# Optimization experiments

Measured on AMD Instinct MI355X. Metric: run time of the kernel, lower is better.

Reference implementation:

```python
import jax, jax.numpy as jnp
import numpy as np
import math

HIDDEN = 384
HEADS = 4
HEAD_DIM = HIDDEN // HEADS
B, T = 8, 2048


def _shift_rel(pos_tensor):
    # pos_tensor: [b, h, t, 2t-1] -> [b, h, t, t] (Transformer-XL shift trick)
    b, h, t, n = pos_tensor.shape
    zero_pad = jnp.zeros((b, h, t, 1), dtype=pos_tensor.dtype)
    padded = jnp.concatenate([zero_pad, pos_tensor], axis=-1)  # [b,h,t,n+1]
    padded = padded.reshape(b, h, n + 1, t)
    shifted = padded[:, :, 1:].reshape(b, h, t, n)
    return shifted[:, :, :, : n // 2 + 1]  # [b,h,t,t]


def setup_inputs() -> dict:
    key = jax.random.key(0)
    ks = jax.random.split(key, 12)
    s = 1.0 / math.sqrt(HIDDEN)
    inp = {
        "hidden_states": jax.random.normal(ks[0], (B, T, HIDDEN), jnp.float32),
        "pos_emb": jax.random.normal(ks[1], (1, 2 * T - 1, HIDDEN), jnp.float32),
        "attention_mask": jnp.ones((B, 1, T), jnp.int32),
        "Wq": jax.random.normal(ks[2], (HIDDEN, HIDDEN), jnp.float32) * s,
        "bq": jnp.zeros((HIDDEN,), jnp.float32),
        "Wk": jax.random.normal(ks[3], (HIDDEN, HIDDEN), jnp.float32) * s,
        "bk": jnp.zeros((HIDDEN,), jnp.float32),
        "Wv": jax.random.normal(ks[4], (HIDDEN, HIDDEN), jnp.float32) * s,
        "bv": jnp.zeros((HIDDEN,), jnp.float32),
        "Wo": jax.random.normal(ks[5], (HIDDEN, HIDDEN), jnp.float32) * s,
        "bo": jnp.zeros((HIDDEN,), jnp.float32),
        "Wpos": jax.random.normal(ks[6], (HIDDEN, HIDDEN), jnp.float32) * s,
        "pos_bias_u": jax.random.normal(ks[7], (HEADS, HEAD_DIM), jnp.float32) * s,
        "pos_bias_v": jax.random.normal(ks[8], (HEADS, HEAD_DIM), jnp.float32) * s,
    }
    return inp


def reference(hidden_states, pos_emb, attention_mask, Wq, bq, Wk, bk, Wv, bv,
              Wo, bo, Wpos, pos_bias_u, pos_bias_v):
    bsz, q_len, _ = hidden_states.shape
    # projections (nn.Linear applies x @ W.T + b; weights here stored as [in, out])
    q = (hidden_states @ Wq + bq).reshape(bsz, q_len, HEADS, HEAD_DIM)
    k = (hidden_states @ Wk + bk).reshape(bsz, q_len, HEADS, HEAD_DIM)
    v = (hidden_states @ Wv + bv).reshape(bsz, q_len, HEADS, HEAD_DIM)
    pos = (pos_emb @ Wpos).reshape(pos_emb.shape[0], -1, HEADS, HEAD_DIM)

    q_u = (q + pos_bias_u).transpose(0, 2, 1, 3)  # [b,h,t,d]
    q_v = (q + pos_bias_v).transpose(0, 2, 1, 3)

    # content score: [b,h,t,t]
    matrix_ac = jnp.einsum('bhqd,bkhd->bhqk', q_u, k)
    # position score: [b,h,t,2t-1] then shift
    matrix_bd = jnp.einsum('bhqd,pnhd->bhqn', q_v, pos)
    matrix_bd = _shift_rel(matrix_bd)

    scores = (matrix_ac + matrix_bd) / math.sqrt(HEAD_DIM)

    mask = (attention_mask[:, None] == 0)  # [b,1,1,t]
    min_val = jnp.finfo(scores.dtype).min
    scores = jnp.where(mask, min_val, scores)
    attn = jax.nn.softmax(scores, axis=-1)
    attn = jnp.where(mask, 0.0, attn)

    out = jnp.einsum('bhqk,bkhd->bqhd', attn, v).reshape(bsz, q_len, HIDDEN)
    return out @ Wo + bo
```

## Files before the change

kernel.cpp:

```cpp
#include <hip/hip_runtime.h>
#include <hip/hip_bf16.h>

#define TSEQ 2048
#define HID 384
#define NHEAD 4
#define HD 96
#define NBATCH 8

using bf16 = __bf16;
typedef bf16 bf16x8 __attribute__((ext_vector_type(8)));
typedef bf16 bf16x4 __attribute__((ext_vector_type(4)));
typedef float f32x4 __attribute__((ext_vector_type(4)));

static __device__ __forceinline__ f32x4 mfma16(bf16x8 a, bf16x8 b, f32x4 c) {
    return __builtin_amdgcn_mfma_f32_16x16x32_bf16(a, b, c, 0, 0, 0);
}

__global__ void k_conv8(const float* __restrict__ src, bf16* __restrict__ dst, int n8) {
    int t = blockIdx.x * 256 + threadIdx.x;
    if (t >= n8) return;
    const float4* s4 = reinterpret_cast<const float4*>(src);
    float4 a = s4[2 * t], b = s4[2 * t + 1];
    bf16x8 o;
    o[0] = (bf16)a.x; o[1] = (bf16)a.y; o[2] = (bf16)a.z; o[3] = (bf16)a.w;
    o[4] = (bf16)b.x; o[5] = (bf16)b.y; o[6] = (bf16)b.z; o[7] = (bf16)b.w;
    *reinterpret_cast<bf16x8*>(dst + 8 * t) = o;
}

__global__ void k_convT(const float* __restrict__ W, bf16* __restrict__ WT) {
    int t = blockIdx.x * 256 + threadIdx.x;
    int n = t / HID, k = t % HID;
    WT[t] = (bf16)W[(size_t)k * HID + n];
}

__launch_bounds__(256, 2)
__global__ void k_proj(const bf16* __restrict__ X, const bf16* __restrict__ P,
                       const bf16* __restrict__ wqT, const bf16* __restrict__ wkT,
                       const bf16* __restrict__ wvT, const bf16* __restrict__ wpT,
                       const float* __restrict__ bq, const float* __restrict__ bk,
                       const float* __restrict__ bv,
                       const float* __restrict__ pbu, const float* __restrict__ pbv,
                       bf16* __restrict__ qu, bf16* __restrict__ qv,
                       bf16* __restrict__ kws, bf16* __restrict__ vt,
                       bf16* __restrict__ pp) {
    __shared__ bf16 wt_lds[96][392];
    const float SC = 0.10206207262f;
    int mat = blockIdx.z;
    int m0 = blockIdx.x * 64;
    if (mat == 3 && m0 >= 4095) return;
    int n0 = blockIdx.y * 96;
    const bf16* A  = (mat == 3) ? P : X;
    const bf16* WT = (mat == 0) ? wqT : (mat == 1) ? wkT : (mat == 2) ? wvT : wpT;
    int tid = threadIdx.x;
    #pragma unroll
    for (int s = 0; s < 18; ++s) {
        int cc = tid + 256 * s;
        int r = cc / 48, ch = cc % 48;
        *reinterpret_cast<int4*>(&wt_lds[r][ch * 8]) =
            *reinterpret_cast<const int4*>(WT + (size_t)(n0 + r) * HID + ch * 8);
    }
    __syncthreads();
    int lane = tid & 63, w = tid >> 6;
    int c = lane & 15, g = lane >> 4;
    int arow = m0 + 16 * w + c;
    if (mat == 3 && arow > 4095) arow = 4095;
    const bf16* Abase = A + (size_t)arow * HID + 8 * g;
    f32x4 acc[6] = {};
    for (int ks = 0; ks < 12; ++ks) {
        bf16x8 a = *reinterpret_cast<const bf16x8*>(Abase + 32 * ks);
        #pragma unroll
        for (int jt = 0; jt < 6; ++jt) {
            bf16x8 b = *reinterpret_cast<const bf16x8*>(&wt_lds[16 * jt + c][32 * ks + 8 * g]);
            acc[jt] = mfma16(a, b, acc[jt]);
        }
    }
    int h = blockIdx.y;
    int rbase = m0 + 16 * w + 4 * g;
    if (mat == 0) {
        #pragma unroll
        for (int jt = 0; jt < 6; ++jt) {
            int n = n0 + 16 * jt + c;
            int d = 16 * jt + c;
            float bb = bq[n], bu = pbu[n], bvv = pbv[n];
            #pragma unroll
            for (int j = 0; j < 4; ++j) {
                int m = rbase + j;
                int b_ = m >> 11, t = m & 2047;
                size_t o = (((size_t)(b_ * NHEAD + h)) * TSEQ + t) * HD + d;
                float q = acc[jt][j] + bb;
                qu[o] = (bf16)((q + bu) * SC);
                qv[o] = (bf16)((q + bvv) * SC);
            }
        }
    } else if (mat == 1) {
        #pragma unroll
        for (int jt = 0; jt < 6; ++jt) {
            int n = n0 + 16 * jt + c;
            int d = 16 * jt + c;
            float bb = bk[n];
            #pragma unroll
            for (int j = 0; j < 4; ++j) {
                int m = rbase + j;
                int b_ = m >> 11, t = m & 2047;
                size_t o = (((size_t)(b_ * NHEAD + h)) * TSEQ + t) * HD + d;
                kws[o] = (bf16)(acc[jt][j] + bb);
            }
        }
    } else if (mat == 2) {
        #pragma unroll
        for (int jt = 0; jt < 6; ++jt) {
            int d = 16 * jt + c;
            float bb = bv[n0 + 16 * jt + c];
            int m = rbase;
            int b_ = m >> 11, t0 = m & 2047;
            size_t o = (((size_t)(b_ * NHEAD + h)) * HD + d) * TSEQ + t0;
            bf16x4 pk;
            #pragma unroll
            for (int j = 0; j < 4; ++j) pk[j] = (bf16)(acc[jt][j] + bb);
            *reinterpret_cast<bf16x4*>(vt + o) = pk;
        }
    } else {
        #pragma unroll
        for (int jt = 0; jt < 6; ++jt) {
            int d = 16 * jt + c;
            #pragma unroll
            for (int j = 0; j < 4; ++j) {
                int m = rbase + j;
                if (m < 4095) {
                    size_t o = ((size_t)h * 4096 + m) * HD + d;
                    pp[o] = (bf16)acc[jt][j];
                }
            }
        }
    }
}

__launch_bounds__(256, 4)
__global__ void k_attn(const bf16* __restrict__ qu, const bf16* __restrict__ qv,
                       const bf16* __restrict__ kws, const bf16* __restrict__ vt,
                       const bf16* __restrict__ pp, const int* __restrict__ mask,
                       bf16* __restrict__ out) {
    __shared__ bf16 k_lds[64][104];
    __shared__ bf16 vt_lds[96][64];
    __shared__ bf16 wp_lds[4][16][104];
    __shared__ float msk_lds[64];

    int bid = blockIdx.x;
    int x = bid & 7, j5 = bid >> 3;
    int h = x & 3;
    int b_ = (x >> 2) * 4 + (j5 >> 5);
    int qb = j5 & 31;
    int bh = b_ * NHEAD + h;
    int q0 = qb * 64;

    int tid = threadIdx.x, lane = tid & 63, w = tid >> 6;
    int c = lane & 15, g = lane >> 4;
    const int n_base0 = TSEQ - 1 - 63 - q0;
    const float L2E = 1.44269504089f;
    int sw = 48 - 16 * w;

    int cc0 = tid, cc1 = tid + 256, cc2 = tid + 512;
    int kr0 = cc0 / 12, kc0 = cc0 % 12;
    int kr1 = cc1 / 12, kc1 = cc1 % 12;
    int kr2 = cc2 / 12, kc2 = cc2 % 12;
    int vr0 = cc0 >> 3, vc0 = cc0 & 7;
    int vr1 = cc1 >> 3, vc1 = cc1 & 7;
    int vr2 = cc2 >> 3, vc2 = cc2 & 7;
    int kO0 = kr0 * HD + kc0 * 8, kO1 = kr1 * HD + kc1 * 8, kO2 = kr2 * HD + kc2 * 8;
    int vO0 = vr0 * TSEQ + vc0 * 8, vO1 = vr1 * TSEQ + vc1 * 8, vO2 = vr2 * TSEQ + vc2 * 8;
    bf16* kP0 = &k_lds[kr0][kc0 * 8];
    bf16* kP1 = &k_lds[kr1][kc1 * 8];
    bf16* kP2 = &k_lds[kr2][kc2 * 8];
    bf16* vP0 = &vt_lds[vr0][(vc0 ^ (vr0 & 7)) * 8];
    bf16* vP1 = &vt_lds[vr1][(vc1 ^ (vr1 & 7)) * 8];
    bf16* vP2 = &vt_lds[vr2][(vc2 ^ (vr2 & 7)) * 8];

    const bf16* kbP = kws + (size_t)bh * TSEQ * HD;
    const bf16* vbP = vt + (size_t)bh * HD * TSEQ;
    const bf16* pbP = pp + (size_t)h * 4096 * HD;
    const int*  mbP = mask + b_ * TSEQ;

    bf16x8 qu_f[3], qv_f[3];
    {
        size_t rowbase = ((size_t)bh * TSEQ + q0 + 16 * w + c) * HD + 8 * g;
        #pragma unroll
        for (int ds = 0; ds < 3; ++ds) {
            qu_f[ds] = *reinterpret_cast<const bf16x8*>(qu + rowbase + 32 * ds);
            qv_f[ds] = *reinterpret_cast<const bf16x8*>(qv + rowbase + 32 * ds);
        }
    }

    f32x4 acc_o[6] = {};
    float mrow = -3.0e38f, lrow = 0.f;

    {
        *reinterpret_cast<int4*>(kP0) = *reinterpret_cast<const int4*>(kbP + kO0);
        *reinterpret_cast<int4*>(kP1) = *reinterpret_cast<const int4*>(kbP + kO1);
        *reinterpret_cast<int4*>(kP2) = *reinterpret_cast<const int4*>(kbP + kO2);
        *reinterpret_cast<int4*>(vP0) = *reinterpret_cast<const int4*>(vbP + vO0);
        *reinterpret_cast<int4*>(vP1) = *reinterpret_cast<const int4*>(vbP + vO1);
        *reinterpret_cast<int4*>(vP2) = *reinterpret_cast<const int4*>(vbP + vO2);
        if (tid < 64) msk_lds[tid] = (mbP[tid] == 0) ? -1e30f : 0.f;
    }
    __syncthreads();

    for (int kt = 0; kt < 32; ++kt) {
        int wbase = n_base0 + 64 * kt + sw;
        {
            f32x4 w0 = {}, w1 = {};
            const bf16* p0 = pbP + (size_t)(wbase + c) * HD + 8 * g;
            const bf16* p1 = pbP + (size_t)(wbase + 16 + c) * HD + 8 * g;
            #pragma unroll
            for (int ds = 0; ds < 3; ++ds) {
                w0 = mfma16(*reinterpret_cast<const bf16x8*>(p0 + 32 * ds), qv_f[ds], w0);
                w1 = mfma16(*reinterpret_cast<const bf16x8*>(p1 + 32 * ds), qv_f[ds], w1);
            }
            #pragma unroll
            for (int j = 0; j < 4; ++j) {
                wp_lds[w][c][4 * g + j + c + 1] = (bf16)w0[j];
                wp_lds[w][c][16 + 4 * g + j + c + 1] = (bf16)w1[j];
            }
        }
        {
            f32x4 w0 = {}, w1 = {};
            const bf16* p0 = pbP + (size_t)(wbase + 32 + c) * HD + 8 * g;
            const bf16* p1 = pbP + (size_t)(wbase + 48 + c) * HD + 8 * g;
            #pragma unroll
            for (int ds = 0; ds < 3; ++ds) {
                w0 = mfma16(*reinterpret_cast<const bf16x8*>(p0 + 32 * ds), qv_f[ds], w0);
                w1 = mfma16(*reinterpret_cast<const bf16x8*>(p1 + 32 * ds), qv_f[ds], w1);
            }
            #pragma unroll
            for (int j = 0; j < 4; ++j) {
                wp_lds[w][c][32 + 4 * g + j + c + 1] = (bf16)w0[j];
                wp_lds[w][c][48 + 4 * g + j + c + 1] = (bf16)w1[j];
            }
        }
        {
            f32x4 w0 = {};
            const bf16* p0 = pbP + (size_t)(wbase + 64 + c) * HD + 8 * g;
            #pragma unroll
            for (int ds = 0; ds < 3; ++ds)
                w0 = mfma16(*reinterpret_cast<const bf16x8*>(p0 + 32 * ds), qv_f[ds], w0);
            #pragma unroll
            for (int j = 0; j < 4; ++j)
                wp_lds[w][c][64 + 4 * g + j + c + 1] = (bf16)w0[j];
        }
        __builtin_amdgcn_s_setprio(1);
        f32x4 acc_s[4] = {};
        #pragma unroll
        for (int ds = 0; ds < 3; ++ds) {
            #pragma unroll
            for (int t = 0; t < 4; ++t) {
                bf16x8 a = *reinterpret_cast<const bf16x8*>(&k_lds[16 * t + c][32 * ds + 8 * g]);
                acc_s[t] = mfma16(a, qu_f[ds], acc_s[t]);
            }
        }
        __builtin_amdgcn_s_setprio(0);
        __threadfence_block();

        #pragma unroll
        for (int t = 0; t < 4; ++t) {
            bf16x4 wv = *reinterpret_cast<const bf16x4*>(&wp_lds[w][c][16 * t + 4 * g + 16]);
            float4 mv = *reinterpret_cast<const float4*>(&msk_lds[16 * t + 4 * g]);
            acc_s[t][0] += (float)wv[0] + mv.x;
            acc_s[t][1] += (float)wv[1] + mv.y;
            acc_s[t][2] += (float)wv[2] + mv.z;
            acc_s[t][3] += (float)wv[3] + mv.w;
        }
        float pm = acc_s[0][0];
        #pragma unroll
        for (int t = 0; t < 4; ++t)
            #pragma unroll
            for (int j = 0; j < 4; ++j) pm = fmaxf(pm, acc_s[t][j]);
        pm = fmaxf(pm, __shfl_xor(pm, 16));
        pm = fmaxf(pm, __shfl_xor(pm, 32));
        if (!__all(pm <= mrow + 8.0f)) {
            float mnew = fmaxf(mrow, pm);
            float alpha = exp2f((mrow - mnew) * L2E);
            mrow = mnew; lrow *= alpha;
            #pragma unroll
            for (int ot = 0; ot < 6; ++ot) acc_o[ot] *= alpha;
        }
        float rs = 0.f;
        #pragma unroll
        for (int t = 0; t < 4; ++t)
            #pragma unroll
            for (int j = 0; j < 4; ++j) {
                float p = exp2f((acc_s[t][j] - mrow) * L2E);
                acc_s[t][j] = p; rs += p;
            }
        rs += __shfl_xor(rs, 16);
        rs += __shfl_xor(rs, 32);
        lrow += rs;

        __threadfence_block();
        #pragma unroll
        for (int t = 0; t < 4; ++t) {
            bf16x4 pk;
            #pragma unroll
            for (int j = 0; j < 4; ++j) pk[j] = (bf16)acc_s[t][j];
            *reinterpret_cast<bf16x4*>(&wp_lds[w][c][16 * t + 4 * g]) = pk;
        }
        __threadfence_block();
        __builtin_amdgcn_s_setprio(1);
        #pragma unroll
        for (int ds = 0; ds < 2; ++ds) {
            bf16x8 pb_ = *reinterpret_cast<const bf16x8*>(&wp_lds[w][c][32 * ds + 8 * g]);
            #pragma unroll
            for (int ot = 0; ot < 6; ++ot) {
                int rr = 16 * ot + c;
                bf16x8 a = *reinterpret_cast<const bf16x8*>(
                    &vt_lds[rr][((4 * ds + g) ^ (rr & 7)) * 8]);
                acc_o[ot] = mfma16(a, pb_, acc_o[ot]);
            }
        }
        __builtin_amdgcn_s_setprio(0);

        __syncthreads();
        {
            int k0n = (kt < 31 ? kt + 1 : 31) * 64;
            const bf16* kb = kbP + (size_t)k0n * HD;
            const bf16* vb = vbP + k0n;
            *reinterpret_cast<int4*>(kP0) = *reinterpret_cast<const int4*>(kb + kO0);
            *reinterpret_cast<int4*>(kP1) = *reinterpret_cast<const int4*>(kb + kO1);
            *reinterpret_cast<int4*>(kP2) = *reinterpret_cast<const int4*>(kb + kO2);
            *reinterpret_cast<int4*>(vP0) = *reinterpret_cast<const int4*>(vb + vO0);
            *reinterpret_cast<int4*>(vP1) = *reinterpret_cast<const int4*>(vb + vO1);
            *reinterpret_cast<int4*>(vP2) = *reinterpret_cast<const int4*>(vb + vO2);
            if (tid < 64) msk_lds[tid] = (mbP[k0n + tid] == 0) ? -1e30f : 0.f;
        }
        __syncthreads();
    }

    float inv = 1.0f / lrow;
    size_t m = (size_t)b_ * TSEQ + q0 + 16 * w + c;
    bf16* ob = out + m * HID + h * HD + 4 * g;
    #pragma unroll
    for (int ot = 0; ot < 6; ++ot) {
        bf16x4 pk;
        #pragma unroll
        for (int j = 0; j < 4; ++j) pk[j] = (bf16)(acc_o[ot][j] * inv);
        *reinterpret_cast<bf16x4*>(&ob[16 * ot]) = pk;
    }
}

__launch_bounds__(256, 2)
__global__ void k_oproj(const bf16* __restrict__ A, const bf16* __restrict__ WT,
                        const float* __restrict__ bias, float* __restrict__ out) {
    __shared__ bf16 wt_lds[96][392];
    int m0 = blockIdx.x * 64, n0 = blockIdx.y * 96;
    int tid = threadIdx.x;
    #pragma unroll
    for (int s = 0; s < 18; ++s) {
        int cc = tid + 256 * s;
        int r = cc / 48, ch = cc % 48;
        *reinterpret_cast<int4*>(&wt_lds[r][ch * 8]) =
            *reinterpret_cast<const int4*>(WT + (size_t)(n0 + r) * HID + ch * 8);
    }
    __syncthreads();
    int lane = tid & 63, w = tid >> 6;
    int c = lane & 15, g = lane >> 4;
    const bf16* Abase = A + (size_t)(m0 + 16 * w + c) * HID + 8 * g;
    f32x4 acc[6] = {};
    for (int ks = 0; ks < 12; ++ks) {
        bf16x8 a = *reinterpret_cast<const bf16x8*>(Abase + 32 * ks);
        #pragma unroll
        for (int jt = 0; jt < 6; ++jt) {
            bf16x8 b = *reinterpret_cast<const bf16x8*>(&wt_lds[16 * jt + c][32 * ks + 8 * g]);
            acc[jt] = mfma16(a, b, acc[jt]);
        }
    }
    int rbase = m0 + 16 * w + 4 * g;
    #pragma unroll
    for (int jt = 0; jt < 6; ++jt) {
        int n = n0 + 16 * jt + c;
        float bb = bias[n];
        #pragma unroll
        for (int j = 0; j < 4; ++j)
            out[(size_t)(rbase + j) * HID + n] = acc[jt][j] + bb;
    }
}

extern "C" void kernel_launch(void* const* d_in, const int* in_sizes, int n_in,
                              void* d_out, int out_size, void* d_ws, size_t ws_size,
                              hipStream_t stream) {
    const float* hs  = (const float*)d_in[0];
    const float* pe  = (const float*)d_in[1];
    const int*   msk = (const int*)d_in[2];
    const float* Wq  = (const float*)d_in[3];
    const float* bq  = (const float*)d_in[4];
    const float* Wk  = (const float*)d_in[5];
    const float* bk  = (const float*)d_in[6];
    const float* Wv  = (const float*)d_in[7];
    const float* bv  = (const float*)d_in[8];
    const float* Wo  = (const float*)d_in[9];
    const float* bo  = (const float*)d_in[10];
    const float* Wp  = (const float*)d_in[11];
    const float* pbu = (const float*)d_in[12];
    const float* pbv = (const float*)d_in[13];

    char* ws = (char*)d_ws;
    size_t off = 0;
    auto alloc = [&](size_t b) { char* p = ws + off; off += (b + 255) & ~(size_t)255; return p; };
    bf16* Xb  = (bf16*)alloc((size_t)16384 * HID * 2);
    bf16* Pb  = (bf16*)alloc((size_t)4096 * HID * 2);
    bf16* wqT = (bf16*)alloc((size_t)HID * HID * 2);
    bf16* wkT = (bf16*)alloc((size_t)HID * HID * 2);
    bf16* wvT = (bf16*)alloc((size_t)HID * HID * 2);
    bf16* woT = (bf16*)alloc((size_t)HID * HID * 2);
    bf16* wpT = (bf16*)alloc((size_t)HID * HID * 2);
    bf16* qu  = (bf16*)alloc((size_t)NBATCH * NHEAD * TSEQ * HD * 2);
    bf16* qv  = (bf16*)alloc((size_t)NBATCH * NHEAD * TSEQ * HD * 2);
    bf16* kws = (bf16*)alloc((size_t)NBATCH * NHEAD * TSEQ * HD * 2);
    bf16* vt  = (bf16*)alloc((size_t)NBATCH * NHEAD * TSEQ * HD * 2);
    bf16* pp  = (bf16*)alloc((size_t)NHEAD * 4096 * HD * 2 + 4096);
    bf16* ao  = (bf16*)alloc((size_t)16384 * HID * 2);

    k_conv8<<<3072, 256, 0, stream>>>(hs, Xb, 786432);
    k_conv8<<<768, 256, 0, stream>>>(pe, Pb, 196560);
    k_convT<<<576, 256, 0, stream>>>(Wq, wqT);
    k_convT<<<576, 256, 0, stream>>>(Wk, wkT);
    k_convT<<<576, 256, 0, stream>>>(Wv, wvT);
    k_convT<<<576, 256, 0, stream>>>(Wo, woT);
    k_convT<<<576, 256, 0, stream>>>(Wp, wpT);
    k_proj<<<dim3(256, 4, 4), 256, 0, stream>>>(Xb, Pb, wqT, wkT, wvT, wpT,
                                                bq, bk, bv, pbu, pbv,
                                                qu, qv, kws, vt, pp);
    k_attn<<<1024, 256, 0, stream>>>(qu, qv, kws, vt, pp, msk, ao);
    k_oproj<<<dim3(256, 4), 256, 0, stream>>>(ao, woT, bo, (float*)d_out);
}
```

Baseline: 318.2 us.

## Read K/V fragments directly from global memory and drop block-level barriers

The attention kernel no longer stages K and V tiles in shared memory. Each wave loads its MFMA operand fragments straight from global memory, which removes both __syncthreads per tile and the shared staging buffers. The position-score MFMA for the tile boundary is reused from the previous iteration, saving one 16-row product per tile. The mask becomes a per-tile ballot applied only when some key is masked, and the shared-memory handoffs use explicit lgkmcnt waits in place of thread fences. The trade-off is redundant global/L2 traffic, since all four waves re-read the same K/V, and more exposed load latency without double buffering.

```diff
diff --git a/kernel.cpp b/kernel.cpp
--- a/kernel.cpp
+++ b/kernel.cpp
@@ -15,6 +15,11 @@
 static __device__ __forceinline__ f32x4 mfma16(bf16x8 a, bf16x8 b, f32x4 c) {
     return __builtin_amdgcn_mfma_f32_16x16x32_bf16(a, b, c, 0, 0, 0);
 }
+
+#define LDS_HANDOFF()                                   \
+    __builtin_amdgcn_sched_barrier(0x7F);               \
+    asm volatile("s_waitcnt lgkmcnt(0)");               \
+    __builtin_amdgcn_sched_barrier(0x7F)
 
 __global__ void k_conv8(const float* __restrict__ src, bf16* __restrict__ dst, int n8) {
     int t = blockIdx.x * 256 + threadIdx.x;
@@ -140,10 +145,7 @@
                        const bf16* __restrict__ kws, const bf16* __restrict__ vt,
                        const bf16* __restrict__ pp, const int* __restrict__ mask,
                        bf16* __restrict__ out) {
-    __shared__ bf16 k_lds[64][104];
-    __shared__ bf16 vt_lds[96][64];
     __shared__ bf16 wp_lds[4][16][104];
-    __shared__ float msk_lds[64];
 
     int bid = blockIdx.x;
     int x = bid & 7, j5 = bid >> 3;
@@ -159,22 +161,6 @@
     const float L2E = 1.44269504089f;
     int sw = 48 - 16 * w;
 
-    int cc0 = tid, cc1 = tid + 256, cc2 = tid + 512;
-    int kr0 = cc0 / 12, kc0 = cc0 % 12;
-    int kr1 = cc1 / 12, kc1 = cc1 % 12;
-    int kr2 = cc2 / 12, kc2 = cc2 % 12;
-    int vr0 = cc0 >> 3, vc0 = cc0 & 7;
-    int vr1 = cc1 >> 3, vc1 = cc1 & 7;
-    int vr2 = cc2 >> 3, vc2 = cc2 & 7;
-    int kO0 = kr0 * HD + kc0 * 8, kO1 = kr1 * HD + kc1 * 8, kO2 = kr2 * HD + kc2 * 8;
-    int vO0 = vr0 * TSEQ + vc0 * 8, vO1 = vr1 * TSEQ + vc1 * 8, vO2 = vr2 * TSEQ + vc2 * 8;
-    bf16* kP0 = &k_lds[kr0][kc0 * 8];
-    bf16* kP1 = &k_lds[kr1][kc1 * 8];
-    bf16* kP2 = &k_lds[kr2][kc2 * 8];
-    bf16* vP0 = &vt_lds[vr0][(vc0 ^ (vr0 & 7)) * 8];
-    bf16* vP1 = &vt_lds[vr1][(vc1 ^ (vr1 & 7)) * 8];
-    bf16* vP2 = &vt_lds[vr2][(vc2 ^ (vr2 & 7)) * 8];
-
     const bf16* kbP = kws + (size_t)bh * TSEQ * HD;
     const bf16* vbP = vt + (size_t)bh * HD * TSEQ;
     const bf16* pbP = pp + (size_t)h * 4096 * HD;
@@ -193,80 +179,83 @@
     f32x4 acc_o[6] = {};
     float mrow = -3.0e38f, lrow = 0.f;
 
+    f32x4 wc = {};
     {
-        *reinterpret_cast<int4*>(kP0) = *reinterpret_cast<const int4*>(kbP + kO0);
-        *reinterpret_cast<int4*>(kP1) = *reinterpret_cast<const int4*>(kbP + kO1);
-        *reinterpret_cast<int4*>(kP2) = *reinterpret_cast<const int4*>(kbP + kO2);
-        *reinterpret_cast<int4*>(vP0) = *reinterpret_cast<const int4*>(vbP + vO0);
-        *reinterpret_cast<int4*>(vP1) = *reinterpret_cast<const int4*>(vbP + vO1);
-        *reinterpret_cast<int4*>(vP2) = *reinterpret_cast<const int4*>(vbP + vO2);
-        if (tid < 64) msk_lds[tid] = (mbP[tid] == 0) ? -1e30f : 0.f;
-    }
-    __syncthreads();
+        const bf16* p0 = pbP + (size_t)(n_base0 + sw + c) * HD + 8 * g;
+        #pragma unroll
+        for (int ds = 0; ds < 3; ++ds)
+            wc = mfma16(*reinterpret_cast<const bf16x8*>(p0 + 32 * ds), qv_f[ds], wc);
+    }
 
     for (int kt = 0; kt < 32; ++kt) {
+        int k0 = kt * 64;
         int wbase = n_base0 + 64 * kt + sw;
+        unsigned long long bm = __ballot(mbP[k0 + lane] != 0);
+
+        #pragma unroll
+        for (int j = 0; j < 4; ++j)
+            wp_lds[w][c][4 * g + j + c + 1] = (bf16)wc[j];
         {
-            f32x4 w0 = {}, w1 = {};
-            const bf16* p0 = pbP + (size_t)(wbase + c) * HD + 8 * g;
+            f32x4 w1 = {}, w2 = {};
             const bf16* p1 = pbP + (size_t)(wbase + 16 + c) * HD + 8 * g;
+            const bf16* p2 = pbP + (size_t)(wbase + 32 + c) * HD + 8 * g;
             #pragma unroll
             for (int ds = 0; ds < 3; ++ds) {
-                w0 = mfma16(*reinterpret_cast<const bf16x8*>(p0 + 32 * ds), qv_f[ds], w0);
                 w1 = mfma16(*reinterpret_cast<const bf16x8*>(p1 + 32 * ds), qv_f[ds], w1);
-            }
-            #pragma unroll
-            for (int j = 0; j < 4; ++j) {
-                wp_lds[w][c][4 * g + j + c + 1] = (bf16)w0[j];
+                w2 = mfma16(*reinterpret_cast<const bf16x8*>(p2 + 32 * ds), qv_f[ds], w2);
+            }
+            #pragma unroll
+            for (int j = 0; j < 4; ++j) {
                 wp_lds[w][c][16 + 4 * g + j + c + 1] = (bf16)w1[j];
+                wp_lds[w][c][32 + 4 * g + j + c + 1] = (bf16)w2[j];
             }
         }
         {
-            f32x4 w0 = {}, w1 = {};
-            const bf16* p0 = pbP + (size_t)(wbase + 32 + c) * HD + 8 * g;
-            const bf16* p1 = pbP + (size_t)(wbase + 48 + c) * HD + 8 * g;
+            f32x4 w3 = {}, w4 = {};
+            const bf16* p3 = pbP + (size_t)(wbase + 48 + c) * HD + 8 * g;
+            const bf16* p4 = pbP + (size_t)(wbase + 64 + c) * HD + 8 * g;
             #pragma unroll
             for (int ds = 0; ds < 3; ++ds) {
-                w0 = mfma16(*reinterpret_cast<const bf16x8*>(p0 + 32 * ds), qv_f[ds], w0);
-                w1 = mfma16(*reinterpret_cast<const bf16x8*>(p1 + 32 * ds), qv_f[ds], w1);
-            }
-            #pragma unroll
-            for (int j = 0; j < 4; ++j) {
-                wp_lds[w][c][32 + 4 * g + j + c + 1] = (bf16)w0[j];
-                wp_lds[w][c][48 + 4 * g + j + c + 1] = (bf16)w1[j];
-            }
-        }
-        {
-            f32x4 w0 = {};
-            const bf16* p0 = pbP + (size_t)(wbase + 64 + c) * HD + 8 * g;
-            #pragma unroll
-            for (int ds = 0; ds < 3; ++ds)
-                w0 = mfma16(*reinterpret_cast<const bf16x8*>(p0 + 32 * ds), qv_f[ds], w0);
-            #pragma unroll
-            for (int j = 0; j < 4; ++j)
-                wp_lds[w][c][64 + 4 * g + j + c + 1] = (bf16)w0[j];
-        }
+                w3 = mfma16(*reinterpret_cast<const bf16x8*>(p3 + 32 * ds), qv_f[ds], w3);
+                w4 = mfma16(*reinterpret_cast<const bf16x8*>(p4 + 32 * ds), qv_f[ds], w4);
+            }
+            #pragma unroll
+            for (int j = 0; j < 4; ++j) {
+                wp_lds[w][c][48 + 4 * g + j + c + 1] = (bf16)w3[j];
+                wp_lds[w][c][64 + 4 * g + j + c + 1] = (bf16)w4[j];
+            }
+            wc = w4;
+        }
+
         __builtin_amdgcn_s_setprio(1);
         f32x4 acc_s[4] = {};
         #pragma unroll
         for (int ds = 0; ds < 3; ++ds) {
             #pragma unroll
             for (int t = 0; t < 4; ++t) {
-                bf16x8 a = *reinterpret_cast<const bf16x8*>(&k_lds[16 * t + c][32 * ds + 8 * g]);
+                bf16x8 a = *reinterpret_cast<const bf16x8*>(
+                    kbP + (size_t)(k0 + 16 * t + c) * HD + 32 * ds + 8 * g);
                 acc_s[t] = mfma16(a, qu_f[ds], acc_s[t]);
             }
         }
         __builtin_amdgcn_s_setprio(0);
-        __threadfence_block();
+
+        LDS_HANDOFF();
 
         #pragma unroll
         for (int t = 0; t < 4; ++t) {
             bf16x4 wv = *reinterpret_cast<const bf16x4*>(&wp_lds[w][c][16 * t + 4 * g + 16]);
-            float4 mv = *reinterpret_cast<const float4*>(&msk_lds[16 * t + 4 * g]);
-            acc_s[t][0] += (float)wv[0] + mv.x;
-            acc_s[t][1] += (float)wv[1] + mv.y;
-            acc_s[t][2] += (float)wv[2] + mv.z;
-            acc_s[t][3] += (float)wv[3] + mv.w;
+            acc_s[t][0] += (float)wv[0];
+            acc_s[t][1] += (float)wv[1];
+            acc_s[t][2] += (float)wv[2];
+            acc_s[t][3] += (float)wv[3];
+        }
+        if (bm != ~0ull) {
+            #pragma unroll
+            for (int t = 0; t < 4; ++t)
+                #pragma unroll
+                for (int j = 0; j < 4; ++j)
+                    if (!((bm >> (16 * t + 4 * g + j)) & 1)) acc_s[t][j] = -3.0e38f;
         }
         float pm = acc_s[0][0];
         #pragma unroll
@@ -294,7 +283,6 @@
         rs += __shfl_xor(rs, 32);
         lrow += rs;
 
-        __threadfence_block();
         #pragma unroll
         for (int t = 0; t < 4; ++t) {
             bf16x4 pk;
@@ -302,35 +290,21 @@
             for (int j = 0; j < 4; ++j) pk[j] = (bf16)acc_s[t][j];
             *reinterpret_cast<bf16x4*>(&wp_lds[w][c][16 * t + 4 * g]) = pk;
         }
-        __threadfence_block();
+
+        LDS_HANDOFF();
+
         __builtin_amdgcn_s_setprio(1);
         #pragma unroll
         for (int ds = 0; ds < 2; ++ds) {
             bf16x8 pb_ = *reinterpret_cast<const bf16x8*>(&wp_lds[w][c][32 * ds + 8 * g]);
             #pragma unroll
             for (int ot = 0; ot < 6; ++ot) {
-                int rr = 16 * ot + c;
                 bf16x8 a = *reinterpret_cast<const bf16x8*>(
-                    &vt_lds[rr][((4 * ds + g) ^ (rr & 7)) * 8]);
+                    vbP + (size_t)(16 * ot + c) * TSEQ + k0 + 32 * ds + 8 * g);
                 acc_o[ot] = mfma16(a, pb_, acc_o[ot]);
             }
         }
         __builtin_amdgcn_s_setprio(0);
-
-        __syncthreads();
-        {
-            int k0n = (kt < 31 ? kt + 1 : 31) * 64;
-            const bf16* kb = kbP + (size_t)k0n * HD;
-            const bf16* vb = vbP + k0n;
-            *reinterpret_cast<int4*>(kP0) = *reinterpret_cast<const int4*>(kb + kO0);
-            *reinterpret_cast<int4*>(kP1) = *reinterpret_cast<const int4*>(kb + kO1);
-            *reinterpret_cast<int4*>(kP2) = *reinterpret_cast<const int4*>(kb + kO2);
-            *reinterpret_cast<int4*>(vP0) = *reinterpret_cast<const int4*>(vb + vO0);
-            *reinterpret_cast<int4*>(vP1) = *reinterpret_cast<const int4*>(vb + vO1);
-            *reinterpret_cast<int4*>(vP2) = *reinterpret_cast<const int4*>(vb + vO2);
-            if (tid < 64) msk_lds[tid] = (mbP[k0n + tid] == 0) ? -1e30f : 0.f;
-        }
-        __syncthreads();
     }
 
     float inv = 1.0f / lrow;
```

After: 439.2 us. +38.0%, slower.
